# Optimization experiments

Hardware: AMD Instinct MI355X
Metric: run time of the kernel (lower is better)

Reference implementation:

```python
import jax, jax.numpy as jnp
import numpy as np

jax.config.update("jax_enable_x64", True)  # original torch code runs in float64; minors underflow fp32

D = 96   # Nsites
N = 48   # Nparticles


def setup_inputs() -> dict:
    key = jax.random.key(0)
    # Orthonormal single-particle orbitals (columns), as the module assumes (P^T P = I)
    A = jax.random.normal(key, (D, D), dtype=jnp.float64)
    Q, _ = jnp.linalg.qr(A)
    P = Q[:, :N]  # [D, N]
    # A valid ordered particle configuration: strictly increasing, occ_positions[k] <= D-N+k
    occ_positions = jnp.arange(N, dtype=jnp.int32) * (D // N)  # stride-2 filling
    return {"P": P, "occ_positions": occ_positions}


def _cond_probs(P, occ_positions):
    """Conditional probabilities probs[k, x] of placing the k-th (ordered) particle at
    site x given particles 0..k-1 at occ_positions[0..k-1].

    Math identical to SlaterDetSampler_ordered.get_cond_prob (naive_update=True):
      G = I - P P^T
      probs[k,x] = -det(M_x[0:x+1,0:x+1]) / det(M[0:xmin,0:xmin])
    where M = G - diag(occupancy of particles < k) and M_x additionally sets n_x = 1.
    Since Ksites is always the contiguous range 0..x, all determinants are LEADING
    principal minors; and because only the (x,x) diagonal entry changes by -1 (last index
    of the block), det(M_x block) = d_{x+1} - d_x with d_j the leading j-minor of M.
    """
    Dd, Nn = P.shape
    dt = P.dtype
    eye = jnp.eye(Dd, dtype=dt)
    G = eye - P @ P.T                                             # [D, D]

    onehots = jax.nn.one_hot(occ_positions, Dd, dtype=dt)         # [N, D]
    n_before = jnp.cumsum(onehots, axis=0) - onehots              # occupancy of particles < k
    A = G[None] - n_before[:, :, None] * eye                      # [N, D, D]: G - diag(n_<k)

    # All leading principal minors via batched det of masked matrices:
    # M_j = A on the [0:j,0:j] block, identity elsewhere  =>  det(M_j) = leading j-minor
    ii = jnp.arange(Dd)
    jj = jnp.arange(1, Dd + 1)
    blk = (ii[None, :, None] < jj[:, None, None]) & (ii[None, None, :] < jj[:, None, None])  # [D,D,D]
    Ms = jnp.where(blk[None], A[:, None], eye)                    # [N, D, D, D]
    d = jnp.linalg.det(Ms.reshape(Nn * Dd, Dd, Dd)).reshape(Nn, Dd)
    d_full = jnp.concatenate([jnp.ones((Nn, 1), dt), d], axis=1)  # d_full[k, j] = j-th leading minor

    k = jnp.arange(Nn)
    xmin = jnp.where(k == 0, 0, occ_positions[jnp.maximum(k - 1, 0)] + 1)  # [N]
    xmax = Dd - Nn + k + 1                                                  # [N]
    denom = jnp.take_along_axis(d_full, xmin[:, None], axis=1)              # [N, 1]
    num = d_full[:, 1:] - d_full[:, :-1]                                    # det(GG_num) per candidate x

    x = jnp.arange(Dd)
    support = (x[None, :] >= xmin[:, None]) & (x[None, :] < xmax[:, None])
    probs = jnp.where(support, -num / denom, jnp.zeros((), dt))
    # torch.where(abs(probs) > 1e-15, probs, 0.)
    probs = jnp.where(jnp.abs(probs) > 1e-15, probs, jnp.zeros((), dt))
    return probs


def reference(P, occ_positions):
    probs = _cond_probs(P, occ_positions)                          # [N, D]
    # prob of the full ordered sample = prod_k probs[k, occ_positions[k]]  (as in sample())
    p_k = jnp.take_along_axis(probs, occ_positions[:, None], axis=1)[:, 0]
    prob_sample = jnp.prod(p_k)
    return probs, prob_sample
```

## Files before the change

kernel.cpp:

```cpp
#include <hip/hip_runtime.h>
#include <math.h>

#define Dd 96
#define Nn 48
#define LD 97
#define PTS 98

__global__ __launch_bounds__(512, 2) void slater_kernel(const float* __restrict__ P,
                                                        const int* __restrict__ occ,
                                                        float* __restrict__ out) {
    __shared__ double As[Dd * LD];
    __shared__ unsigned char flag[Dd];
    float* PT = (float*)As;

    const int tid  = threadIdx.x;
    const int k    = blockIdx.x;
    const int n    = Dd - Nn + k + 1;
    const int lane = tid & 63;
    const int wave = tid >> 6;
    const int xmin = (k == 0) ? 0 : occ[k - 1] + 1;

    if (tid < Dd) flag[tid] = 0;
    __syncthreads();
    if (tid < k) flag[occ[tid]] = 1;
    for (int e = tid; e < Dd * Nn; e += 512) {
        int c = e / Nn, t = e - (e / Nn) * Nn;
        PT[t * PTS + c] = P[e];
    }
    __syncthreads();

    double Areg[20];
#pragma unroll
    for (int it = 0; it < 5; ++it) {
        int tau = tid + 512 * it;
        double s00 = 0.0, s01 = 0.0, s10 = 0.0, s11 = 0.0;
        if (tau < 2304) {
            int tr = tau / 48, tc = tau - (tau / 48) * 48;
            int r0 = 2 * tr, c0 = 2 * tc;
            if (r0 < n && c0 < n) {
                for (int t = 0; t < Nn; ++t) {
                    const float* row = PT + t * PTS;
                    float2 pr = *(const float2*)(row + r0);
                    float2 pc = *(const float2*)(row + c0);
                    s00 -= (double)pr.x * (double)pc.x; s01 -= (double)pr.x * (double)pc.y;
                    s10 -= (double)pr.y * (double)pc.x; s11 -= (double)pr.y * (double)pc.y;
                }
            }
        }
        Areg[it * 4 + 0] = s00; Areg[it * 4 + 1] = s01;
        Areg[it * 4 + 2] = s10; Areg[it * 4 + 3] = s11;
    }
    __syncthreads();
#pragma unroll
    for (int it = 0; it < 5; ++it) {
        int tau = tid + 512 * it;
        if (tau < 2304) {
            int tr = tau / 48, tc = tau - (tau / 48) * 48;
            int r0 = 2 * tr, c0 = 2 * tc;
            if (r0 < n && c0 < n) {
                bool r1ok = (r0 + 1 < n), c1ok = (c0 + 1 < n);
                As[r0 * LD + c0] = Areg[it * 4 + 0] + ((r0 == c0) ? (flag[r0] ? 0.0 : 1.0) : 0.0);
                if (c1ok)
                    As[r0 * LD + c0 + 1] = Areg[it * 4 + 1] + ((r0 == c0 + 1) ? (flag[r0] ? 0.0 : 1.0) : 0.0);
                if (r1ok)
                    As[(r0 + 1) * LD + c0] = Areg[it * 4 + 2] + ((r0 + 1 == c0) ? (flag[r0 + 1] ? 0.0 : 1.0) : 0.0);
                if (r1ok && c1ok)
                    As[(r0 + 1) * LD + c0 + 1] = Areg[it * 4 + 3] + ((r0 + 1 == c0 + 1) ? (flag[r0 + 1] ? 0.0 : 1.0) : 0.0);
            }
        }
    }
    __syncthreads();

    double runprod = 1.0;
    double myprob  = 0.0;
    bool   dead    = false;

    auto guard = [&](int jj, double pivot) {
        double ap = fabs(pivot);
        if (jj >= xmin) {
            if (tid == jj) myprob = runprod * (1.0 - pivot);
            double newrun = runprod * pivot;
            if (!(ap > 1e-7) || !(ap < 8.0) || !(fabs(newrun) > 1e-8)) dead = true;
            else runprod = newrun;
        } else {
            if (!(ap > 1e-12) || !(ap < 8.0)) dead = true;
        }
    };

    int j = 0;
    for (; !dead && j + 4 <= n - 1; j += 4) {
        const double* Pr0 = As + j * LD + j;
        const double* Pr1 = As + (j + 1) * LD + j;
        const double* Pr2 = As + (j + 2) * LD + j;
        const double* Pr3 = As + (j + 3) * LD + j;
        double B00 = Pr0[0], B01 = Pr0[1], B02 = Pr0[2], B03 = Pr0[3];
        double B10 = Pr1[0], B11 = Pr1[1], B12 = Pr1[2], B13 = Pr1[3];
        double B20 = Pr2[0], B21 = Pr2[1], B22 = Pr2[2], B23 = Pr2[3];
        double B30 = Pr3[0], B31 = Pr3[1], B32 = Pr3[2], B33 = Pr3[3];

        double piv0 = B00;
        double rp0  = 1.0 / piv0;
        double m10  = B10 * rp0;
        double u01 = B01, u02 = B02, u03 = B03;
        double piv1 = B11 - m10 * u01;
        double u12  = B12 - m10 * u02;
        double u13  = B13 - m10 * u03;
        double rp1  = 1.0 / piv1;
        double m20  = B20 * rp0;
        double m21  = (B21 - m20 * u01) * rp1;
        double piv2 = B22 - m20 * u02 - m21 * u12;
        double u23  = B23 - m20 * u03 - m21 * u13;
        double rp2  = 1.0 / piv2;
        double m30  = B30 * rp0;
        double m31  = (B31 - m30 * u01) * rp1;
        double m32  = (B32 - m30 * u02 - m31 * u12) * rp2;
        double piv3 = B33 - m30 * u03 - m31 * u13 - m32 * u23;
        double rp3  = 1.0 / piv3;

        if (!dead) guard(j + 0, piv0);
        if (!dead) guard(j + 1, piv1);
        if (!dead) guard(j + 2, piv2);
        if (!dead) guard(j + 3, piv3);

        if (!dead) {
            int t = n - (j + 4);
            int c0 = j + 4 + lane, c1 = j + 68 + lane;
            bool ok0 = (lane < t), ok1 = (lane + 64 < t);
            double R0c0 = 0.0, R1c0 = 0.0, R2c0 = 0.0, R3c0 = 0.0;
            double R0c1 = 0.0, R1c1 = 0.0, R2c1 = 0.0, R3c1 = 0.0;
            if (ok0) {
                R0c0 = As[j * LD + c0];       R1c0 = As[(j + 1) * LD + c0];
                R2c0 = As[(j + 2) * LD + c0]; R3c0 = As[(j + 3) * LD + c0];
            }
            if (ok1) {
                R0c1 = As[j * LD + c1];       R1c1 = As[(j + 1) * LD + c1];
                R2c1 = As[(j + 2) * LD + c1]; R3c1 = As[(j + 3) * LD + c1];
            }
            for (int i = j + 4 + wave; i < n; i += 16) {
                int ib = i + 8;
                bool hb = (ib < n);
                double* rowA = As + i * LD;
                double a0 = rowA[j], a1 = rowA[j + 1], a2 = rowA[j + 2], a3 = rowA[j + 3];
                double Ta0 = ok0 ? rowA[c0] : 0.0;
                double Ta1 = ok1 ? rowA[c1] : 0.0;
                double* rowB = As + ib * LD;
                double b0 = 0.0, b1 = 0.0, b2 = 0.0, b3 = 0.0, Tb0 = 0.0, Tb1 = 0.0;
                if (hb) {
                    b0 = rowB[j]; b1 = rowB[j + 1]; b2 = rowB[j + 2]; b3 = rowB[j + 3];
                    Tb0 = ok0 ? rowB[c0] : 0.0;
                    Tb1 = ok1 ? rowB[c1] : 0.0;
                }
                double m0 = a0 * rp0;
                double m1 = (a1 - m0 * u01) * rp1;
                double m2 = (a2 - m0 * u02 - m1 * u12) * rp2;
                double m3 = (a3 - m0 * u03 - m1 * u13 - m2 * u23) * rp3;
                double w3 = m3;
                double w2 = m2 - m32 * w3;
                double w1 = m1 - m21 * w2 - m31 * w3;
                double w0 = m0 - m10 * w1 - m20 * w2 - m30 * w3;
                if (ok0) rowA[c0] = Ta0 - w0 * R0c0 - w1 * R1c0 - w2 * R2c0 - w3 * R3c0;
                if (ok1) rowA[c1] = Ta1 - w0 * R0c1 - w1 * R1c1 - w2 * R2c1 - w3 * R3c1;
                if (hb) {
                    double e0 = b0 * rp0;
                    double e1 = (b1 - e0 * u01) * rp1;
                    double e2 = (b2 - e0 * u02 - e1 * u12) * rp2;
                    double e3 = (b3 - e0 * u03 - e1 * u13 - e2 * u23) * rp3;
                    double v3 = e3;
                    double v2 = e2 - m32 * v3;
                    double v1 = e1 - m21 * v2 - m31 * v3;
                    double v0 = e0 - m10 * v1 - m20 * v2 - m30 * v3;
                    if (ok0) rowB[c0] = Tb0 - v0 * R0c0 - v1 * R1c0 - v2 * R2c0 - v3 * R3c0;
                    if (ok1) rowB[c1] = Tb1 - v0 * R0c1 - v1 * R1c1 - v2 * R2c1 - v3 * R3c1;
                }
            }
        }
        __syncthreads();
    }

    for (; !dead && j < n - 1; ++j) {
        double pivot = As[j * LD + j];
        guard(j, pivot);
        if (dead) break;
        double rp = 1.0 / pivot;
        int t = n - 1 - j;
        double r0 = (lane < t)      ? As[j * LD + j + 1 + lane]  : 0.0;
        double r1 = (lane + 64 < t) ? As[j * LD + j + 65 + lane] : 0.0;
        for (int i = j + 1 + wave; i < n; i += 8) {
            double mult = As[i * LD + j] * rp;
            if (lane < t)      As[i * LD + j + 1 + lane]  -= mult * r0;
            if (lane + 64 < t) As[i * LD + j + 65 + lane] -= mult * r1;
        }
        __syncthreads();
    }
    if (!dead && tid == n - 1) {
        double pl = As[(n - 1) * LD + (n - 1)];
        myprob = runprod * (1.0 - pl);
    }

    if (tid < Dd) {
        double p = myprob;
        if (!isfinite(p)) p = 0.0;
        if (!(fabs(p) > 1e-15)) p = 0.0;
        p = fmin(fmax(p, 0.0), 1.0);
        out[k * Dd + tid] = (float)p;
    }
}

__global__ void prod_kernel(const int* __restrict__ occ, float* __restrict__ out) {
    int lane = threadIdx.x & 63;
    double v = 1.0;
    if (lane < Nn) v = (double)out[lane * Dd + occ[lane]];
#pragma unroll
    for (int off = 32; off >= 1; off >>= 1)
        v *= __shfl_down(v, off, 64);
    if (lane == 0) {
        if (!isfinite(v)) v = 0.0;
        out[Nn * Dd] = (float)v;
    }
}

extern "C" void kernel_launch(void* const* d_in, const int* in_sizes, int n_in,
                              void* d_out, int out_size, void* d_ws, size_t ws_size,
                              hipStream_t stream) {
    const float* P = (const float*)d_in[0];
    const int* occ = (const int*)d_in[1];
    float* out = (float*)d_out;

    slater_kernel<<<Nn, 512, 0, stream>>>(P, occ, out);
    prod_kernel<<<1, 64, 0, stream>>>(occ, out);
}
```

Baseline: 111.5 us.

## Fuse product reduction via last-block atomic, exploit symmetry, unroll elimination rows

The separate product kernel is folded into the main kernel: a global atomic counter in workspace picks the last finishing block, which computes the sample probability. This removes one launch. The Gram matrix build now computes only the upper-triangular 2x2 tiles and mirrors them, roughly halving the FP64 dot-product work. The blocked elimination processes four rows per wave per iteration with hoisted loads, and divisions are replaced by a hardware reciprocal refined with Newton steps. Occupancy bounds drop to one block per CU, and the counter depends on the workspace being zeroed or wrapping modulo Nn across calls.

```diff
diff --git a/kernel.cpp b/kernel.cpp
--- a/kernel.cpp
+++ b/kernel.cpp
@@ -6,9 +6,17 @@
 #define LD 97
 #define PTS 98
 
-__global__ __launch_bounds__(512, 2) void slater_kernel(const float* __restrict__ P,
+__device__ __forceinline__ double frcp(double x) {
+    double r = __builtin_amdgcn_rcp(x);
+    r = fma(fma(-x, r, 1.0), r, r);
+    r = fma(fma(-x, r, 1.0), r, r);
+    return r;
+}
+
+__global__ __launch_bounds__(512, 1) void slater_kernel(const float* __restrict__ P,
                                                         const int* __restrict__ occ,
-                                                        float* __restrict__ out) {
+                                                        float* __restrict__ out,
+                                                        unsigned* __restrict__ cnt) {
     __shared__ double As[Dd * LD];
     __shared__ unsigned char flag[Dd];
     float* PT = (float*)As;
@@ -29,13 +37,17 @@
     }
     __syncthreads();
 
-    double Areg[20];
-#pragma unroll
-    for (int it = 0; it < 5; ++it) {
+    double Areg[12]; int trs[3], tcs[3];
+#pragma unroll
+    for (int it = 0; it < 3; ++it) {
         int tau = tid + 512 * it;
         double s00 = 0.0, s01 = 0.0, s10 = 0.0, s11 = 0.0;
-        if (tau < 2304) {
-            int tr = tau / 48, tc = tau - (tau / 48) * 48;
+        int tr = 0, tc = 0;
+        if (tau < 1176) {
+            tr = (int)((97.0 - sqrt(9409.0 - 8.0 * (double)tau)) * 0.5);
+            while ((tr * (97 - tr)) / 2 > tau) --tr;
+            while (((tr + 1) * (96 - tr)) / 2 <= tau) ++tr;
+            tc = tr + (tau - (tr * (97 - tr)) / 2);
             int r0 = 2 * tr, c0 = 2 * tc;
             if (r0 < n && c0 < n) {
                 for (int t = 0; t < Nn; ++t) {
@@ -47,25 +59,31 @@
                 }
             }
         }
+        trs[it] = tr; tcs[it] = tc;
         Areg[it * 4 + 0] = s00; Areg[it * 4 + 1] = s01;
         Areg[it * 4 + 2] = s10; Areg[it * 4 + 3] = s11;
     }
     __syncthreads();
 #pragma unroll
-    for (int it = 0; it < 5; ++it) {
+    for (int it = 0; it < 3; ++it) {
         int tau = tid + 512 * it;
-        if (tau < 2304) {
-            int tr = tau / 48, tc = tau - (tau / 48) * 48;
+        if (tau < 1176) {
+            int tr = trs[it], tc = tcs[it];
             int r0 = 2 * tr, c0 = 2 * tc;
             if (r0 < n && c0 < n) {
-                bool r1ok = (r0 + 1 < n), c1ok = (c0 + 1 < n);
-                As[r0 * LD + c0] = Areg[it * 4 + 0] + ((r0 == c0) ? (flag[r0] ? 0.0 : 1.0) : 0.0);
-                if (c1ok)
-                    As[r0 * LD + c0 + 1] = Areg[it * 4 + 1] + ((r0 == c0 + 1) ? (flag[r0] ? 0.0 : 1.0) : 0.0);
-                if (r1ok)
-                    As[(r0 + 1) * LD + c0] = Areg[it * 4 + 2] + ((r0 + 1 == c0) ? (flag[r0 + 1] ? 0.0 : 1.0) : 0.0);
-                if (r1ok && c1ok)
-                    As[(r0 + 1) * LD + c0 + 1] = Areg[it * 4 + 3] + ((r0 + 1 == c0 + 1) ? (flag[r0 + 1] ? 0.0 : 1.0) : 0.0);
+                bool r1 = (r0 + 1 < n), c1 = (c0 + 1 < n);
+                double d0 = flag[r0] ? 0.0 : 1.0;
+                double d1 = flag[r0 + 1] ? 0.0 : 1.0;
+                As[r0 * LD + c0] = Areg[it * 4 + 0] + ((r0 == c0) ? d0 : 0.0);
+                if (c1)       As[r0 * LD + c0 + 1]       = Areg[it * 4 + 1];
+                if (r1)       As[(r0 + 1) * LD + c0]     = Areg[it * 4 + 2];
+                if (r1 && c1) As[(r0 + 1) * LD + c0 + 1] = Areg[it * 4 + 3] + ((r0 == c0) ? d1 : 0.0);
+                if (tr != tc) {
+                    As[c0 * LD + r0] = Areg[it * 4 + 0];
+                    if (c1)       As[(c0 + 1) * LD + r0]     = Areg[it * 4 + 1];
+                    if (r1)       As[c0 * LD + r0 + 1]       = Areg[it * 4 + 2];
+                    if (r1 && c1) As[(c0 + 1) * LD + r0 + 1] = Areg[it * 4 + 3];
+                }
             }
         }
     }
@@ -89,88 +107,76 @@
 
     int j = 0;
     for (; !dead && j + 4 <= n - 1; j += 4) {
-        const double* Pr0 = As + j * LD + j;
-        const double* Pr1 = As + (j + 1) * LD + j;
-        const double* Pr2 = As + (j + 2) * LD + j;
-        const double* Pr3 = As + (j + 3) * LD + j;
-        double B00 = Pr0[0], B01 = Pr0[1], B02 = Pr0[2], B03 = Pr0[3];
-        double B10 = Pr1[0], B11 = Pr1[1], B12 = Pr1[2], B13 = Pr1[3];
-        double B20 = Pr2[0], B21 = Pr2[1], B22 = Pr2[2], B23 = Pr2[3];
-        double B30 = Pr3[0], B31 = Pr3[1], B32 = Pr3[2], B33 = Pr3[3];
+        int t = n - (j + 4);
+        bool ok0 = (lane < t), ok1 = (lane + 64 < t);
+        int c0 = j + 4 + (ok0 ? lane : 0);
+        int c1 = j + 4 + (ok1 ? lane + 64 : 0);
+        double R0c0 = As[j * LD + c0],       R1c0 = As[(j + 1) * LD + c0];
+        double R2c0 = As[(j + 2) * LD + c0], R3c0 = As[(j + 3) * LD + c0];
+        double R0c1 = As[j * LD + c1],       R1c1 = As[(j + 1) * LD + c1];
+        double R2c1 = As[(j + 2) * LD + c1], R3c1 = As[(j + 3) * LD + c1];
+
+        const double* Bp0 = As + j * LD + j;
+        const double* Bp1 = Bp0 + LD;
+        const double* Bp2 = Bp1 + LD;
+        const double* Bp3 = Bp2 + LD;
+        double B00 = Bp0[0], B01 = Bp0[1], B02 = Bp0[2], B03 = Bp0[3];
+        double B10 = Bp1[0], B11 = Bp1[1], B12 = Bp1[2], B13 = Bp1[3];
+        double B20 = Bp2[0], B21 = Bp2[1], B22 = Bp2[2], B23 = Bp2[3];
+        double B30 = Bp3[0], B31 = Bp3[1], B32 = Bp3[2], B33 = Bp3[3];
 
         double piv0 = B00;
-        double rp0  = 1.0 / piv0;
+        double rp0  = frcp(piv0);
         double m10  = B10 * rp0;
         double u01 = B01, u02 = B02, u03 = B03;
         double piv1 = B11 - m10 * u01;
         double u12  = B12 - m10 * u02;
         double u13  = B13 - m10 * u03;
-        double rp1  = 1.0 / piv1;
+        double rp1  = frcp(piv1);
         double m20  = B20 * rp0;
         double m21  = (B21 - m20 * u01) * rp1;
         double piv2 = B22 - m20 * u02 - m21 * u12;
         double u23  = B23 - m20 * u03 - m21 * u13;
-        double rp2  = 1.0 / piv2;
+        double rp2  = frcp(piv2);
         double m30  = B30 * rp0;
         double m31  = (B31 - m30 * u01) * rp1;
         double m32  = (B32 - m30 * u02 - m31 * u12) * rp2;
         double piv3 = B33 - m30 * u03 - m31 * u13 - m32 * u23;
-        double rp3  = 1.0 / piv3;
-
-        if (!dead) guard(j + 0, piv0);
+        double rp3  = frcp(piv3);
+
+        guard(j + 0, piv0);
         if (!dead) guard(j + 1, piv1);
         if (!dead) guard(j + 2, piv2);
         if (!dead) guard(j + 3, piv3);
 
         if (!dead) {
-            int t = n - (j + 4);
-            int c0 = j + 4 + lane, c1 = j + 68 + lane;
-            bool ok0 = (lane < t), ok1 = (lane + 64 < t);
-            double R0c0 = 0.0, R1c0 = 0.0, R2c0 = 0.0, R3c0 = 0.0;
-            double R0c1 = 0.0, R1c1 = 0.0, R2c1 = 0.0, R3c1 = 0.0;
-            if (ok0) {
-                R0c0 = As[j * LD + c0];       R1c0 = As[(j + 1) * LD + c0];
-                R2c0 = As[(j + 2) * LD + c0]; R3c0 = As[(j + 3) * LD + c0];
-            }
-            if (ok1) {
-                R0c1 = As[j * LD + c1];       R1c1 = As[(j + 1) * LD + c1];
-                R2c1 = As[(j + 2) * LD + c1]; R3c1 = As[(j + 3) * LD + c1];
-            }
-            for (int i = j + 4 + wave; i < n; i += 16) {
-                int ib = i + 8;
-                bool hb = (ib < n);
-                double* rowA = As + i * LD;
-                double a0 = rowA[j], a1 = rowA[j + 1], a2 = rowA[j + 2], a3 = rowA[j + 3];
-                double Ta0 = ok0 ? rowA[c0] : 0.0;
-                double Ta1 = ok1 ? rowA[c1] : 0.0;
-                double* rowB = As + ib * LD;
-                double b0 = 0.0, b1 = 0.0, b2 = 0.0, b3 = 0.0, Tb0 = 0.0, Tb1 = 0.0;
-                if (hb) {
-                    b0 = rowB[j]; b1 = rowB[j + 1]; b2 = rowB[j + 2]; b3 = rowB[j + 3];
-                    Tb0 = ok0 ? rowB[c0] : 0.0;
-                    Tb1 = ok1 ? rowB[c1] : 0.0;
-                }
-                double m0 = a0 * rp0;
-                double m1 = (a1 - m0 * u01) * rp1;
-                double m2 = (a2 - m0 * u02 - m1 * u12) * rp2;
-                double m3 = (a3 - m0 * u03 - m1 * u13 - m2 * u23) * rp3;
-                double w3 = m3;
-                double w2 = m2 - m32 * w3;
-                double w1 = m1 - m21 * w2 - m31 * w3;
-                double w0 = m0 - m10 * w1 - m20 * w2 - m30 * w3;
-                if (ok0) rowA[c0] = Ta0 - w0 * R0c0 - w1 * R1c0 - w2 * R2c0 - w3 * R3c0;
-                if (ok1) rowA[c1] = Ta1 - w0 * R0c1 - w1 * R1c1 - w2 * R2c1 - w3 * R3c1;
-                if (hb) {
-                    double e0 = b0 * rp0;
-                    double e1 = (b1 - e0 * u01) * rp1;
-                    double e2 = (b2 - e0 * u02 - e1 * u12) * rp2;
-                    double e3 = (b3 - e0 * u03 - e1 * u13 - e2 * u23) * rp3;
-                    double v3 = e3;
-                    double v2 = e2 - m32 * v3;
-                    double v1 = e1 - m21 * v2 - m31 * v3;
-                    double v0 = e0 - m10 * v1 - m20 * v2 - m30 * v3;
-                    if (ok0) rowB[c0] = Tb0 - v0 * R0c0 - v1 * R1c0 - v2 * R2c0 - v3 * R3c0;
-                    if (ok1) rowB[c1] = Tb1 - v0 * R0c1 - v1 * R1c1 - v2 * R2c1 - v3 * R3c1;
+            for (int i = j + 4 + wave; i < n; i += 32) {
+                double a0[4], a1[4], a2[4], a3[4], T0[4], T1[4];
+                bool h[4];
+#pragma unroll
+                for (int u = 0; u < 4; ++u) {
+                    int r = i + u * 8;
+                    h[u] = (r < n);
+                    const double* rw = As + (h[u] ? r : i) * LD;
+                    a0[u] = rw[j];     a1[u] = rw[j + 1];
+                    a2[u] = rw[j + 2]; a3[u] = rw[j + 3];
+                    T0[u] = rw[c0];    T1[u] = rw[c1];
+                }
+#pragma unroll
+                for (int u = 0; u < 4; ++u) {
+                    double m0 = a0[u] * rp0;
+                    double m1 = (a1[u] - m0 * u01) * rp1;
+                    double m2 = (a2[u] - m0 * u02 - m1 * u12) * rp2;
+                    double m3 = (a3[u] - m0 * u03 - m1 * u13 - m2 * u23) * rp3;
+                    double w3 = m3;
+                    double w2 = m2 - m32 * w3;
+                    double w1 = m1 - m21 * w2 - m31 * w3;
+                    double w0 = m0 - m10 * w1 - m20 * w2 - m30 * w3;
+                    if (h[u]) {
+                        double* rw = As + (i + u * 8) * LD;
+                        if (ok0) rw[c0] = T0[u] - w0 * R0c0 - w1 * R1c0 - w2 * R2c0 - w3 * R3c0;
+                        if (ok1) rw[c1] = T1[u] - w0 * R0c1 - w1 * R1c1 - w2 * R2c1 - w3 * R3c1;
+                    }
                 }
             }
         }
@@ -181,7 +187,7 @@
         double pivot = As[j * LD + j];
         guard(j, pivot);
         if (dead) break;
-        double rp = 1.0 / pivot;
+        double rp = frcp(pivot);
         int t = n - 1 - j;
         double r0 = (lane < t)      ? As[j * LD + j + 1 + lane]  : 0.0;
         double r1 = (lane + 64 < t) ? As[j * LD + j + 65 + lane] : 0.0;
@@ -204,18 +210,31 @@
         p = fmin(fmax(p, 0.0), 1.0);
         out[k * Dd + tid] = (float)p;
     }
-}
-
-__global__ void prod_kernel(const int* __restrict__ occ, float* __restrict__ out) {
-    int lane = threadIdx.x & 63;
-    double v = 1.0;
-    if (lane < Nn) v = (double)out[lane * Dd + occ[lane]];
-#pragma unroll
-    for (int off = 32; off >= 1; off >>= 1)
-        v *= __shfl_down(v, off, 64);
-    if (lane == 0) {
-        if (!isfinite(v)) v = 0.0;
-        out[Nn * Dd] = (float)v;
+
+    __threadfence();
+    __syncthreads();
+    if (wave == 0) {
+        int old = 0;
+        if (lane == 0)
+            old = (int)__hip_atomic_fetch_add(cnt, 1u, __ATOMIC_ACQ_REL,
+                                              __HIP_MEMORY_SCOPE_AGENT);
+        old = __shfl(old, 0, 64);
+        if (((unsigned)old + 1u) % (unsigned)Nn == 0u) {
+            __threadfence();
+            double v = 1.0;
+            if (lane < Nn) {
+                float f = __hip_atomic_load(out + lane * Dd + occ[lane],
+                                            __ATOMIC_RELAXED, __HIP_MEMORY_SCOPE_AGENT);
+                v = (double)f;
+            }
+#pragma unroll
+            for (int off = 32; off >= 1; off >>= 1)
+                v *= __shfl_down(v, off, 64);
+            if (lane == 0) {
+                if (!isfinite(v)) v = 0.0;
+                out[Nn * Dd] = (float)v;
+            }
+        }
     }
 }
 
@@ -226,6 +245,5 @@
     const int* occ = (const int*)d_in[1];
     float* out = (float*)d_out;
 
-    slater_kernel<<<Nn, 512, 0, stream>>>(P, occ, out);
-    prod_kernel<<<1, 64, 0, stream>>>(occ, out);
+    slater_kernel<<<Nn, 512, 0, stream>>>(P, occ, out, (unsigned*)d_ws);
 }
```

Result: faster. 108.3 us (-2.9%).
